# Kernel tuning notes

Measured on AMD Instinct MI355X. Metric: run time of the kernel, lower is better.

The kernel has to match this reference:

```python
import jax, jax.numpy as jnp
import numpy as np

EPS = 1e-12  # torch F.normalize eps

def _l2norm(x):
    # F.normalize(x, p=2, dim=-1): x / max(||x||_2, eps)
    n = jnp.sqrt(jnp.sum(x * x, axis=-1, keepdims=True))
    return x / jnp.maximum(n, EPS)

def setup_inputs() -> dict:
    key = jax.random.key(0)
    k1, k2, k3 = jax.random.split(key, 3)
    B, N, D = 8, 8192, 512
    return {
        "s": jax.random.normal(k1, (B, N, D), dtype=jnp.float32),
        "h_rl": jax.random.normal(k2, (B, N, D), dtype=jnp.float32),
        "h_fk": jax.random.normal(k3, (B, N, D), dtype=jnp.float32),
    }

def reference(s, h_rl, h_fk):
    # diagonal(bmm(s, h^T)) == row-wise dot product; compute it directly
    s_n = _l2norm(s)
    sc_rl = jnp.sum(s_n * _l2norm(h_rl), axis=-1)  # [B, N]
    sc_fk = jnp.sum(s_n * _l2norm(h_fk), axis=-1)  # [B, N]
    return jnp.concatenate((sc_rl, sc_fk), axis=1)  # [B, 2N]
```

## Files before the change

kernel.cpp:

```cpp
#include <hip/hip_runtime.h>

#define DIM 512
#define NPB 8192

typedef float f4 __attribute__((ext_vector_type(4)));

__device__ __forceinline__ float dot4(f4 u, f4 v) {
    f4 p = u * v;
    return p.x + p.y + p.z + p.w;
}

__global__ __launch_bounds__(256) void disc_kernel(
    const float* __restrict__ s,
    const float* __restrict__ hrl,
    const float* __restrict__ hfk,
    float* __restrict__ out,
    int n_rows) {
    int row  = (blockIdx.x * blockDim.x + threadIdx.x) >> 6;
    int lane = threadIdx.x & 63;
    if (row >= n_rows) return;

    size_t base = (size_t)row * DIM;
    const f4* sp = (const f4*)(s   + base);
    const f4* ap = (const f4*)(hrl + base);
    const f4* bp = (const f4*)(hfk + base);

    f4 s0 = sp[lane], s1 = sp[lane + 64];
    f4 a0 = ap[lane], a1 = ap[lane + 64];
    f4 b0 = bp[lane], b1 = bp[lane + 64];

    float ss = dot4(s0, s0) + dot4(s1, s1);
    float aa = dot4(a0, a0) + dot4(a1, a1);
    float bb = dot4(b0, b0) + dot4(b1, b1);
    float sa = dot4(s0, a0) + dot4(s1, a1);
    float sb = dot4(s0, b0) + dot4(s1, b1);

    #pragma unroll
    for (int off = 32; off > 0; off >>= 1) {
        ss += __shfl_xor(ss, off, 64);
        aa += __shfl_xor(aa, off, 64);
        bb += __shfl_xor(bb, off, 64);
        sa += __shfl_xor(sa, off, 64);
        sb += __shfl_xor(sb, off, 64);
    }

    if (lane == 0) {
        const float eps = 1e-12f;
        float ns = fmaxf(sqrtf(ss), eps);
        float na = fmaxf(sqrtf(aa), eps);
        float nb = fmaxf(sqrtf(bb), eps);
        int bidx = row >> 13;
        int n    = row & (NPB - 1);
        size_t obase = (size_t)bidx * (2 * NPB) + n;
        out[obase]       = sa / (ns * na);
        out[obase + NPB] = sb / (ns * nb);
    }
}

extern "C" void kernel_launch(void* const* d_in, const int* in_sizes, int n_in,
                              void* d_out, int out_size, void* d_ws, size_t ws_size,
                              hipStream_t stream) {
    const float* s   = (const float*)d_in[0];
    const float* hrl = (const float*)d_in[1];
    const float* hfk = (const float*)d_in[2];
    float* out = (float*)d_out;

    int n_rows = in_sizes[0] / DIM;
    int threads = 256;
    int blocks = (n_rows + 3) / 4;
    disc_kernel<<<blocks, threads, 0, stream>>>(s, hrl, hfk, out, n_rows);
}
```

Baseline: 343.5 us.

## Use persistent waves with two rows per iteration and register double-buffered prefetch

Replaces the one-wave-per-row launch with a fixed grid of persistent waves. Each wave processes two consecutive rows per iteration and prefetches the next pair into registers while reducing the current pair. This is meant to keep more loads in flight per wave and amortise launch and tail overhead on a bandwidth-bound streaming kernel. It raises register pressure (24 f4 buffers), and the iteration count assumes n_rows divides evenly by the wave count times two, so it has no remainder handling.

After: 351.7 us. +2.4%, slower.

```diff
diff --git a/kernel.cpp b/kernel.cpp
--- a/kernel.cpp
+++ b/kernel.cpp
@@ -2,6 +2,10 @@
 
 #define DIM 512
 #define NPB 8192
+#define NBLK 1024
+#define TPB 256
+#define NWAVES (NBLK * TPB / 64)
+#define RPI 2
 
 typedef float f4 __attribute__((ext_vector_type(4)));
 
@@ -10,50 +14,83 @@
     return p.x + p.y + p.z + p.w;
 }
 
-__global__ __launch_bounds__(256) void disc_kernel(
+__global__ __launch_bounds__(TPB, 4) void disc_kernel(
     const float* __restrict__ s,
     const float* __restrict__ hrl,
     const float* __restrict__ hfk,
     float* __restrict__ out,
     int n_rows) {
-    int row  = (blockIdx.x * blockDim.x + threadIdx.x) >> 6;
+    int wid  = (blockIdx.x * blockDim.x + threadIdx.x) >> 6;
     int lane = threadIdx.x & 63;
-    if (row >= n_rows) return;
 
-    size_t base = (size_t)row * DIM;
-    const f4* sp = (const f4*)(s   + base);
-    const f4* ap = (const f4*)(hrl + base);
-    const f4* bp = (const f4*)(hfk + base);
+    const int iters = n_rows / (NWAVES * RPI);
 
-    f4 s0 = sp[lane], s1 = sp[lane + 64];
-    f4 a0 = ap[lane], a1 = ap[lane + 64];
-    f4 b0 = bp[lane], b1 = bp[lane + 64];
+    size_t base = (size_t)wid * RPI * DIM;
+    const size_t step = (size_t)NWAVES * RPI * DIM;
 
-    float ss = dot4(s0, s0) + dot4(s1, s1);
-    float aa = dot4(a0, a0) + dot4(a1, a1);
-    float bb = dot4(b0, b0) + dot4(b1, b1);
-    float sa = dot4(s0, a0) + dot4(s1, a1);
-    float sb = dot4(s0, b0) + dot4(s1, b1);
+    f4 cur[12], nxt[12];
 
-    #pragma unroll
-    for (int off = 32; off > 0; off >>= 1) {
-        ss += __shfl_xor(ss, off, 64);
-        aa += __shfl_xor(aa, off, 64);
-        bb += __shfl_xor(bb, off, 64);
-        sa += __shfl_xor(sa, off, 64);
-        sb += __shfl_xor(sb, off, 64);
-    }
+    auto load_pair = [&](size_t b, f4* dst) {
+        const f4* sp = (const f4*)(s   + b);
+        const f4* ap = (const f4*)(hrl + b);
+        const f4* bp = (const f4*)(hfk + b);
+        dst[0]  = sp[lane];       dst[1]  = sp[lane + 64];
+        dst[2]  = ap[lane];       dst[3]  = ap[lane + 64];
+        dst[4]  = bp[lane];       dst[5]  = bp[lane + 64];
+        dst[6]  = sp[lane + 128]; dst[7]  = sp[lane + 192];
+        dst[8]  = ap[lane + 128]; dst[9]  = ap[lane + 192];
+        dst[10] = bp[lane + 128]; dst[11] = bp[lane + 192];
+    };
 
-    if (lane == 0) {
-        const float eps = 1e-12f;
-        float ns = fmaxf(sqrtf(ss), eps);
-        float na = fmaxf(sqrtf(aa), eps);
-        float nb = fmaxf(sqrtf(bb), eps);
-        int bidx = row >> 13;
-        int n    = row & (NPB - 1);
-        size_t obase = (size_t)bidx * (2 * NPB) + n;
-        out[obase]       = sa / (ns * na);
-        out[obase + NPB] = sb / (ns * nb);
+    load_pair(base, cur);
+
+    for (int it = 0; it < iters; ++it) {
+        if (it + 1 < iters) {
+            load_pair(base + step, nxt);
+        }
+        __builtin_amdgcn_sched_barrier(0);
+
+        float v[10];
+        v[0] = dot4(cur[0], cur[0]) + dot4(cur[1], cur[1]);
+        v[1] = dot4(cur[2], cur[2]) + dot4(cur[3], cur[3]);
+        v[2] = dot4(cur[4], cur[4]) + dot4(cur[5], cur[5]);
+        v[3] = dot4(cur[0], cur[2]) + dot4(cur[1], cur[3]);
+        v[4] = dot4(cur[0], cur[4]) + dot4(cur[1], cur[5]);
+        v[5] = dot4(cur[6], cur[6])  + dot4(cur[7], cur[7]);
+        v[6] = dot4(cur[8], cur[8])  + dot4(cur[9], cur[9]);
+        v[7] = dot4(cur[10], cur[10]) + dot4(cur[11], cur[11]);
+        v[8] = dot4(cur[6], cur[8])  + dot4(cur[7], cur[9]);
+        v[9] = dot4(cur[6], cur[10]) + dot4(cur[7], cur[11]);
+
+        #pragma unroll
+        for (int off = 32; off > 0; off >>= 1) {
+            #pragma unroll
+            for (int k = 0; k < 10; ++k) v[k] += __shfl_xor(v[k], off, 64);
+        }
+
+        if (lane == 0) {
+            const float eps = 1e-12f;
+            int row0 = (int)(base / DIM);
+            int bidx = row0 >> 13;
+            int n0   = row0 & (NPB - 1);
+            size_t obase = (size_t)bidx * (2 * NPB) + n0;
+
+            float ns0 = fmaxf(sqrtf(v[0]), eps);
+            float na0 = fmaxf(sqrtf(v[1]), eps);
+            float nb0 = fmaxf(sqrtf(v[2]), eps);
+            out[obase]           = v[3] / (ns0 * na0);
+            out[obase + NPB]     = v[4] / (ns0 * nb0);
+
+            float ns1 = fmaxf(sqrtf(v[5]), eps);
+            float na1 = fmaxf(sqrtf(v[6]), eps);
+            float nb1 = fmaxf(sqrtf(v[7]), eps);
+            out[obase + 1]       = v[8] / (ns1 * na1);
+            out[obase + NPB + 1] = v[9] / (ns1 * nb1);
+        }
+
+        #pragma unroll
+        for (int k = 0; k < 12; ++k) cur[k] = nxt[k];
+        base += step;
     }
 }
 
@@ -66,7 +103,5 @@
     float* out = (float*)d_out;
 
     int n_rows = in_sizes[0] / DIM;
-    int threads = 256;
-    int blocks = (n_rows + 3) / 4;
-    disc_kernel<<<blocks, threads, 0, stream>>>(s, hrl, hfk, out, n_rows);
+    disc_kernel<<<NBLK, TPB, 0, stream>>>(s, hrl, hfk, out, n_rows);
 }
```
